# Optimization experiments

Hardware: AMD Instinct MI355X
Metric: run time of the kernel (lower is better)

## Reference

```python
import jax, jax.numpy as jnp
import numpy as np

N_NODES = 100000
N_EDGES = 1600000
IN_SIZE = 128
HIDDEN = 128
OUT_SIZE = 64


def setup_inputs() -> dict:
    key = jax.random.key(0)
    k = jax.random.split(key, 8)
    feat = jax.random.normal(k[0], (N_NODES, IN_SIZE), dtype=jnp.float32)
    src = jax.random.randint(k[1], (N_EDGES,), 0, N_NODES, dtype=jnp.int32)
    dst = jax.random.randint(k[2], (N_EDGES,), 0, N_NODES, dtype=jnp.int32)
    # fc_neigh weights for the two SAGEConv layers (stored as [in, out])
    W1 = jax.random.normal(k[3], (IN_SIZE, HIDDEN), dtype=jnp.float32) / np.sqrt(IN_SIZE)
    b1 = jnp.zeros((HIDDEN,), dtype=jnp.float32)
    W2 = jax.random.normal(k[4], (HIDDEN, OUT_SIZE), dtype=jnp.float32) / np.sqrt(HIDDEN)
    b2 = jnp.zeros((OUT_SIZE,), dtype=jnp.float32)
    return {"feat": feat, "W1": W1, "b1": b1, "W2": W2, "b2": b2,
            "src": src, "dst": dst}


def _sage_gcn(h, src, dst, W, b):
    # DGL SAGEConv with aggregator_type='gcn':
    #   neigh = segment_sum over incoming edges of src features
    #   h_neigh = (neigh + h_self) / (in_degree + 1)
    #   out = h_neigh @ W + b   (fc_self is not used for 'gcn')
    neigh = jax.ops.segment_sum(h[src], dst, num_segments=N_NODES)  # [N, d]
    deg = jax.ops.segment_sum(jnp.ones((src.shape[0],), dtype=h.dtype), dst,
                              num_segments=N_NODES)                 # [N]
    h_neigh = (neigh + h) / (deg + 1.0)[:, None]
    return h_neigh @ W + b


def reference(feat, W1, b1, W2, b2, src, dst):
    # dropout(p=0.0) is identity; activation between layers only
    h = _sage_gcn(feat, src, dst, W1, b1)
    h = jax.nn.relu(h)
    h = _sage_gcn(h, src, dst, W2, b2)
    return h
```

## Files before the change

kernel.cpp:

```cpp
#include <hip/hip_runtime.h>

#define NNODES 100000
#define NEDGES 1600000
#define BSHIFT 7
#define NB 782
#define CAP 2560
#define EBLOCKS 391
#define GEMM_BLOCKS 1563

typedef _Float16 f16;
typedef _Float16 v8h __attribute__((ext_vector_type(8)));
typedef float v4f __attribute__((ext_vector_type(4)));

#if __has_builtin(__builtin_amdgcn_cvt_f32_ubyte0)
#define CVTB0(u) __builtin_amdgcn_cvt_f32_ubyte0(u)
#define CVTB1(u) __builtin_amdgcn_cvt_f32_ubyte1(u)
#define CVTB2(u) __builtin_amdgcn_cvt_f32_ubyte2(u)
#define CVTB3(u) __builtin_amdgcn_cvt_f32_ubyte3(u)
#else
#define CVTB0(u) ((float)((u) & 0xFFu))
#define CVTB1(u) ((float)(((u) >> 8) & 0xFFu))
#define CVTB2(u) ((float)(((u) >> 16) & 0xFFu))
#define CVTB3(u) ((float)((u) >> 24))
#endif

__device__ inline void acc8(float s, uint2 u, float* a) {
    a[0] = fmaf(s, CVTB0(u.x), a[0]);
    a[1] = fmaf(s, CVTB1(u.x), a[1]);
    a[2] = fmaf(s, CVTB2(u.x), a[2]);
    a[3] = fmaf(s, CVTB3(u.x), a[3]);
    a[4] = fmaf(s, CVTB0(u.y), a[4]);
    a[5] = fmaf(s, CVTB1(u.y), a[5]);
    a[6] = fmaf(s, CVTB2(u.y), a[6]);
    a[7] = fmaf(s, CVTB3(u.y), a[7]);
}

__global__ __launch_bounds__(256) void init_k(int* __restrict__ bcur,
                                              const float* __restrict__ W1,
                                              f16* __restrict__ W1t,
                                              const float* __restrict__ W2,
                                              f16* __restrict__ W2t) {
    int t = blockIdx.x * 256 + threadIdx.x;
    if (t < NB) bcur[t] = t * CAP;
    int u = t - 1024;
    if (u >= 0) {
        if (u < 128 * 128) {
            int k = u >> 7, n = u & 127;
            W1t[n * 128 + k] = (f16)W1[k * 128 + n];
        } else if (u < 128 * 128 + 128 * 64) {
            int v = u - 128 * 128;
            int k = v >> 6, n = v & 63;
            W2t[n * 128 + k] = (f16)W2[k * 64 + n];
        }
    }
}

__global__ __launch_bounds__(256) void scatter_gemm1(
    const int* __restrict__ src, const int* __restrict__ dst,
    int* __restrict__ bcur, int* __restrict__ ebuf,
    const float* __restrict__ feat, const f16* __restrict__ W1t,
    unsigned char* __restrict__ z1, float* __restrict__ sc1) {
    constexpr int PITCH = 136;
    __shared__ __align__(16) char smem[128 * PITCH * 2];
    int tid = threadIdx.x;

    if (blockIdx.x < EBLOCKS) {
        int* h = (int*)smem;
        int* base_s = ((int*)smem) + 1024;
        for (int i = tid; i < NB; i += 256) h[i] = 0;
        __syncthreads();
        int base = blockIdx.x * 4096;
        int d[16], sv[16];
        for (int k = 0; k < 16; k++) {
            int e = base + k * 256 + tid;
            if (e < NEDGES) {
                d[k] = dst[e];
                sv[k] = src[e];
                atomicAdd(&h[d[k] >> BSHIFT], 1);
            } else {
                d[k] = -1;
            }
        }
        __syncthreads();
        for (int i = tid; i < NB; i += 256) {
            int c = h[i];
            if (c) base_s[i] = atomicAdd(&bcur[i], c);
            h[i] = 0;
        }
        __syncthreads();
        for (int k = 0; k < 16; k++) {
            if (d[k] >= 0) {
                int b = d[k] >> BSHIFT;
                int slot = atomicAdd(&h[b], 1);
                ebuf[base_s[b] + slot] = sv[k] | ((d[k] & 127) << 24);
            }
        }
        return;
    }

    f16* wlds = (f16*)smem;
    for (int c = tid; c < 128 * 16; c += 256) {
        int n = c >> 4;
        int kc = c & 15;
        *(v8h*)&wlds[n * PITCH + kc * 8] = *(const v8h*)&W1t[n * 128 + kc * 8];
    }
    __syncthreads();

    int wave = tid >> 6, lane = tid & 63, quad = lane >> 4, l16 = lane & 15;
    int m0 = (blockIdx.x - EBLOCKS) * 64 + wave * 16;
    if (m0 >= NNODES) return;

    v8h a[4];
    const float* arow = feat + (long)(m0 + l16) * 128 + quad * 8;
#pragma unroll
    for (int kb = 0; kb < 4; kb++) {
        float4 f0 = *(const float4*)(arow + kb * 32);
        float4 f1 = *(const float4*)(arow + kb * 32 + 4);
        v8h t = {(f16)f0.x, (f16)f0.y, (f16)f0.z, (f16)f0.w,
                 (f16)f1.x, (f16)f1.y, (f16)f1.z, (f16)f1.w};
        a[kb] = t;
    }

    v4f acc[8];
#pragma unroll
    for (int nt = 0; nt < 8; nt++) {
        v4f c4 = {0.f, 0.f, 0.f, 0.f};
        const f16* brow = &wlds[(nt * 16 + l16) * PITCH + quad * 8];
#pragma unroll
        for (int kb = 0; kb < 4; kb++) {
            v8h b = *(const v8h*)(brow + kb * 32);
            c4 = __builtin_amdgcn_mfma_f32_16x16x32_f16(a[kb], b, c4, 0, 0, 0);
        }
        acc[nt] = c4;
    }

#pragma unroll
    for (int r = 0; r < 4; r++) {
        float m = 0.f;
#pragma unroll
        for (int nt = 0; nt < 8; nt++) m = fmaxf(m, fabsf(acc[nt][r]));
        m = fmaxf(m, __shfl_xor(m, 1));
        m = fmaxf(m, __shfl_xor(m, 2));
        m = fmaxf(m, __shfl_xor(m, 4));
        m = fmaxf(m, __shfl_xor(m, 8));
        int row = m0 + quad * 4 + r;
        float rs = (m > 0.f) ? 127.f / m : 0.f;
        if (l16 == 0) sc1[row] = (m > 0.f) ? m / 127.f : 0.f;
#pragma unroll
        for (int nt = 0; nt < 8; nt++) {
            int qv = (int)rintf(acc[nt][r] * rs) + 128;
            z1[(long)row * 128 + nt * 16 + l16] = (unsigned char)qv;
        }
    }
}

__global__ __launch_bounds__(256) void fill_bucket(const int* __restrict__ ebuf,
                                                   const int* __restrict__ bcur,
                                                   const float* __restrict__ sc1,
                                                   int* __restrict__ begs,
                                                   int* __restrict__ ends,
                                                   int2* __restrict__ csr8) {
    __shared__ int lc[128];
    __shared__ int ls[256];
    int b = blockIdx.x;
    int tid = threadIdx.x;
    if (tid < 128) lc[tid] = 0;
    __syncthreads();
    int ebeg = b * CAP;
    int eend = bcur[b];
    for (int e = ebeg + tid; e < eend; e += 256)
        atomicAdd(&lc[((unsigned)ebuf[e]) >> 24], 1);
    __syncthreads();
    int cnt = (tid < 128) ? lc[tid] : 0;
    ls[tid] = cnt;
    __syncthreads();
    for (int off = 1; off < 256; off <<= 1) {
        int t = (tid >= off) ? ls[tid - off] : 0;
        __syncthreads();
        ls[tid] += t;
        __syncthreads();
    }
    int excl = ls[tid] - cnt;
    int node = (b << BSHIFT) + tid;
    if (tid < 128 && node < NNODES) {
        begs[node] = ebeg + excl;
        ends[node] = ebeg + excl + cnt;
    }
    if (tid < 128) { ls[tid] = excl; lc[tid] = 0; }
    __syncthreads();
    for (int e = ebeg + tid; e < eend; e += 256) {
        int p = ebuf[e];
        int dloc = ((unsigned)p) >> 24;
        int s = p & 0xFFFFFF;
        int slot = atomicAdd(&lc[dloc], 1);
        csr8[ebeg + ls[dloc] + slot] = make_int2(s, __float_as_int(sc1[s]));
    }
}

__global__ __launch_bounds__(256, 8) void gather128_h1(
    const unsigned char* __restrict__ z,
    const float* __restrict__ sc,
    const int2* __restrict__ csr8,
    const int* __restrict__ begs, const int* __restrict__ ends,
    const float* __restrict__ b1,
    f16* __restrict__ h1)
{
    int tid = threadIdx.x;
    int c = tid & 15;
    int node = blockIdx.x * 16 + (tid >> 4);

    int beg = begs[node];
    int end = ends[node];

    unsigned coff = (unsigned)c << 3;

    float a[8];
#pragma unroll
    for (int j = 0; j < 8; j++) a[j] = 0.f;
    float ssum = 0.f;

    {
        float s = sc[node];
        uint2 u = *(const uint2*)(z + (((unsigned)node) << 7) + coff);
        ssum += s;
        acc8(s, u, a);
    }

    int e = beg;
    while (__any(e < end)) {
        int2 q0 = {0, 0}, q1 = {0, 0}, q2 = {0, 0}, q3 = {0, 0};
        int2 q4 = {0, 0}, q5 = {0, 0}, q6 = {0, 0}, q7 = {0, 0};
        if (e     < end) q0 = csr8[e];
        if (e + 1 < end) q1 = csr8[e + 1];
        if (e + 2 < end) q2 = csr8[e + 2];
        if (e + 3 < end) q3 = csr8[e + 3];
        if (e + 4 < end) q4 = csr8[e + 4];
        if (e + 5 < end) q5 = csr8[e + 5];
        if (e + 6 < end) q6 = csr8[e + 6];
        if (e + 7 < end) q7 = csr8[e + 7];
        uint2 u0 = make_uint2(0, 0), u1 = make_uint2(0, 0);
        uint2 u2 = make_uint2(0, 0), u3 = make_uint2(0, 0);
        uint2 u4 = make_uint2(0, 0), u5 = make_uint2(0, 0);
        uint2 u6 = make_uint2(0, 0), u7 = make_uint2(0, 0);
        if (e     < end) u0 = *(const uint2*)(z + (((unsigned)q0.x) << 7) + coff);
        if (e + 1 < end) u1 = *(const uint2*)(z + (((unsigned)q1.x) << 7) + coff);
        if (e + 2 < end) u2 = *(const uint2*)(z + (((unsigned)q2.x) << 7) + coff);
        if (e + 3 < end) u3 = *(const uint2*)(z + (((unsigned)q3.x) << 7) + coff);
        if (e + 4 < end) u4 = *(const uint2*)(z + (((unsigned)q4.x) << 7) + coff);
        if (e + 5 < end) u5 = *(const uint2*)(z + (((unsigned)q5.x) << 7) + coff);
        if (e + 6 < end) u6 = *(const uint2*)(z + (((unsigned)q6.x) << 7) + coff);
        if (e + 7 < end) u7 = *(const uint2*)(z + (((unsigned)q7.x) << 7) + coff);
        float s0 = __int_as_float(q0.y), s1 = __int_as_float(q1.y);
        float s2 = __int_as_float(q2.y), s3 = __int_as_float(q3.y);
        float s4 = __int_as_float(q4.y), s5 = __int_as_float(q5.y);
        float s6 = __int_as_float(q6.y), s7 = __int_as_float(q7.y);
        ssum += ((s0 + s1) + (s2 + s3)) + ((s4 + s5) + (s6 + s7));
        acc8(s0, u0, a); acc8(s1, u1, a); acc8(s2, u2, a); acc8(s3, u3, a);
        acc8(s4, u4, a); acc8(s5, u5, a); acc8(s6, u6, a); acc8(s7, u7, a);
        e += 8;
    }

    {
        float base = 128.f * ssum;
        float inv = 1.0f / (float)(end - beg + 1);
        float4 bb0 = ((const float4*)b1)[c * 2];
        float4 bb1 = ((const float4*)b1)[c * 2 + 1];
        v8h o = {(f16)fmaxf((a[0] - base) * inv + bb0.x, 0.f),
                 (f16)fmaxf((a[1] - base) * inv + bb0.y, 0.f),
                 (f16)fmaxf((a[2] - base) * inv + bb0.z, 0.f),
                 (f16)fmaxf((a[3] - base) * inv + bb0.w, 0.f),
                 (f16)fmaxf((a[4] - base) * inv + bb1.x, 0.f),
                 (f16)fmaxf((a[5] - base) * inv + bb1.y, 0.f),
                 (f16)fmaxf((a[6] - base) * inv + bb1.z, 0.f),
                 (f16)fmaxf((a[7] - base) * inv + bb1.w, 0.f)};
        *(v8h*)&h1[(long)node * 128 + c * 8] = o;
    }
}

__global__ __launch_bounds__(256) void gemm2_k(
    const f16* __restrict__ h1,
    const f16* __restrict__ W2t,
    unsigned char* __restrict__ z2,
    float* __restrict__ sc2)
{
    constexpr int PITCH = 136;
    __shared__ f16 wlds[64 * PITCH];
    int tid = threadIdx.x;
    for (int c = tid; c < 64 * 16; c += 256) {
        int n = c >> 4;
        int kc = c & 15;
        *(v8h*)&wlds[n * PITCH + kc * 8] = *(const v8h*)&W2t[n * 128 + kc * 8];
    }
    __syncthreads();

    int wave = tid >> 6, lane = tid & 63, quad = lane >> 4, l16 = lane & 15;
    int m0 = blockIdx.x * 64 + wave * 16;
    if (m0 >= NNODES) return;

    v8h a[4];
    const f16* arow = h1 + (long)(m0 + l16) * 128 + quad * 8;
#pragma unroll
    for (int kb = 0; kb < 4; kb++) a[kb] = *(const v8h*)(arow + kb * 32);

    v4f acc[4];
#pragma unroll
    for (int nt = 0; nt < 4; nt++) {
        v4f c4 = {0.f, 0.f, 0.f, 0.f};
        const f16* brow = &wlds[(nt * 16 + l16) * PITCH + quad * 8];
#pragma unroll
        for (int kb = 0; kb < 4; kb++) {
            v8h b = *(const v8h*)(brow + kb * 32);
            c4 = __builtin_amdgcn_mfma_f32_16x16x32_f16(a[kb], b, c4, 0, 0, 0);
        }
        acc[nt] = c4;
    }

#pragma unroll
    for (int r = 0; r < 4; r++) {
        float m = 0.f;
#pragma unroll
        for (int nt = 0; nt < 4; nt++) m = fmaxf(m, fabsf(acc[nt][r]));
        m = fmaxf(m, __shfl_xor(m, 1));
        m = fmaxf(m, __shfl_xor(m, 2));
        m = fmaxf(m, __shfl_xor(m, 4));
        m = fmaxf(m, __shfl_xor(m, 8));
        int row = m0 + quad * 4 + r;
        float rs = (m > 0.f) ? 127.f / m : 0.f;
        if (l16 == 0) sc2[row] = (m > 0.f) ? m / 127.f : 0.f;
#pragma unroll
        for (int nt = 0; nt < 4; nt++) {
            int qv = (int)rintf(acc[nt][r] * rs) + 128;
            z2[(long)row * 64 + nt * 16 + l16] = (unsigned char)qv;
        }
    }
}

__global__ __launch_bounds__(256, 8) void gather64(
    const unsigned char* __restrict__ z, const float* __restrict__ sc,
    const int2* __restrict__ csr8,
    const int* __restrict__ begs, const int* __restrict__ ends,
    const float* __restrict__ bias, float4* __restrict__ out) {
    int tid = threadIdx.x;
    int lane = tid & 63;
    int c = lane & 7;
    int node = blockIdx.x * 32 + (tid >> 3);

    int beg = begs[node];
    int end = ends[node];

    unsigned coff = (unsigned)c << 3;

    float a[8];
#pragma unroll
    for (int j = 0; j < 8; j++) a[j] = 0.f;
    float ssum = 0.f;

    {
        float s = sc[node];
        uint2 u = *(const uint2*)(z + (((unsigned)node) << 6) + coff);
        ssum += s;
        acc8(s, u, a);
    }

    int e = beg;
    while (__any(e < end)) {
        float s0 = 0.f, s1 = 0.f, s2 = 0.f, s3 = 0.f;
        float s4 = 0.f, s5 = 0.f, s6 = 0.f, s7 = 0.f;
        uint2 u0 = make_uint2(0, 0), u1 = make_uint2(0, 0);
        uint2 u2 = make_uint2(0, 0), u3 = make_uint2(0, 0);
        uint2 u4 = make_uint2(0, 0), u5 = make_uint2(0, 0);
        uint2 u6 = make_uint2(0, 0), u7 = make_uint2(0, 0);
        if (e     < end) { int i = csr8[e    ].x; s0 = sc[i]; u0 = *(const uint2*)(z + (((unsigned)i) << 6) + coff); }
        if (e + 1 < end) { int i = csr8[e + 1].x; s1 = sc[i]; u1 = *(const uint2*)(z + (((unsigned)i) << 6) + coff); }
        if (e + 2 < end) { int i = csr8[e + 2].x; s2 = sc[i]; u2 = *(const uint2*)(z + (((unsigned)i) << 6) + coff); }
        if (e + 3 < end) { int i = csr8[e + 3].x; s3 = sc[i]; u3 = *(const uint2*)(z + (((unsigned)i) << 6) + coff); }
        if (e + 4 < end) { int i = csr8[e + 4].x; s4 = sc[i]; u4 = *(const uint2*)(z + (((unsigned)i) << 6) + coff); }
        if (e + 5 < end) { int i = csr8[e + 5].x; s5 = sc[i]; u5 = *(const uint2*)(z + (((unsigned)i) << 6) + coff); }
        if (e + 6 < end) { int i = csr8[e + 6].x; s6 = sc[i]; u6 = *(const uint2*)(z + (((unsigned)i) << 6) + coff); }
        if (e + 7 < end) { int i = csr8[e + 7].x; s7 = sc[i]; u7 = *(const uint2*)(z + (((unsigned)i) << 6) + coff); }
        ssum += ((s0 + s1) + (s2 + s3)) + ((s4 + s5) + (s6 + s7));
        acc8(s0, u0, a); acc8(s1, u1, a); acc8(s2, u2, a); acc8(s3, u3, a);
        acc8(s4, u4, a); acc8(s5, u5, a); acc8(s6, u6, a); acc8(s7, u7, a);
        e += 8;
    }

    {
        float base = 128.f * ssum;
        float inv = 1.0f / (float)(end - beg + 1);
        float4 b0 = ((const float4*)bias)[c * 2];
        float4 b1v = ((const float4*)bias)[c * 2 + 1];
        out[(long)node * 16 + c * 2] =
            make_float4((a[0] - base) * inv + b0.x, (a[1] - base) * inv + b0.y,
                        (a[2] - base) * inv + b0.z, (a[3] - base) * inv + b0.w);
        out[(long)node * 16 + c * 2 + 1] =
            make_float4((a[4] - base) * inv + b1v.x, (a[5] - base) * inv + b1v.y,
                        (a[6] - base) * inv + b1v.z, (a[7] - base) * inv + b1v.w);
    }
}

extern "C" void kernel_launch(void* const* d_in, const int* in_sizes, int n_in,
                              void* d_out, int out_size, void* d_ws, size_t ws_size,
                              hipStream_t stream) {
    const float* feat = (const float*)d_in[0];
    const float* W1   = (const float*)d_in[1];
    const float* b1   = (const float*)d_in[2];
    const float* W2   = (const float*)d_in[3];
    const float* b2   = (const float*)d_in[4];
    const int*   src  = (const int*)d_in[5];
    const int*   dst  = (const int*)d_in[6];
    float* out = (float*)d_out;

    char* ws = (char*)d_ws;
    int* bcur = (int*)(ws + 0x0000000);
    int* begs = (int*)(ws + 0x0001000);
    int* ends = (int*)(ws + 0x0063000);
    int* ebuf = (int*)(ws + 0x00C5000);
    int2* csr8 = (int2*)(ws + 0x0900000);
    unsigned char* z1 = (unsigned char*)(ws + 0x1900000);
    float* sc1 = (float*)(ws + 0x2600000);
    f16* h1   = (f16*)(ws + 0x2700000);
    unsigned char* z2 = (unsigned char*)(ws + 0x4100000);
    float* sc2 = (float*)(ws + 0x4800000);
    f16* W1t  = (f16*)(ws + 0x4900000);
    f16* W2t  = (f16*)(ws + 0x4910000);

    init_k<<<100, 256, 0, stream>>>(bcur, W1, W1t, W2, W2t);

    scatter_gemm1<<<EBLOCKS + GEMM_BLOCKS, 256, 0, stream>>>(src, dst, bcur, ebuf,
                                                             feat, W1t, z1, sc1);

    fill_bucket<<<NB, 256, 0, stream>>>(ebuf, bcur, sc1, begs, ends, csr8);

    gather128_h1<<<NNODES / 16, 256, 0, stream>>>(z1, sc1, csr8, begs, ends,
                                                  b1, h1);

    gemm2_k<<<GEMM_BLOCKS, 256, 0, stream>>>(h1, W2t, z2, sc2);

    gather64<<<3125, 256, 0, stream>>>(z2, sc2, csr8, begs, ends, b2,
                                       (float4*)out);
}
```

Measured before the change: 249.9 us.

## Switch int8 quantization from per-row to per-column scales with integer gather accumulation

Replaces per-row int8 scales with per-column scales found through a global atomicMax over each GEMM's output. The scale can then be applied once after aggregation, so the gathers sum packed bytes with plain integer adds instead of float FMAs. The CSR shrinks from int2 to int4, and scale loads per edge are gone. In exchange, the GEMMs now write fp16 intermediates and separate quantize passes (merged into fill_quant, plus quant_z2) add extra memory traffic and launches. Per-column scales may also lose accuracy compared with per-row scales.

```diff
diff --git a/kernel.cpp b/kernel.cpp
--- a/kernel.cpp
+++ b/kernel.cpp
@@ -7,41 +7,31 @@
 #define CAP 2560
 #define EBLOCKS 391
 #define GEMM_BLOCKS 1563
+#define QBLOCKS 6250
 
 typedef _Float16 f16;
 typedef _Float16 v8h __attribute__((ext_vector_type(8)));
 typedef float v4f __attribute__((ext_vector_type(4)));
 
-#if __has_builtin(__builtin_amdgcn_cvt_f32_ubyte0)
-#define CVTB0(u) __builtin_amdgcn_cvt_f32_ubyte0(u)
-#define CVTB1(u) __builtin_amdgcn_cvt_f32_ubyte1(u)
-#define CVTB2(u) __builtin_amdgcn_cvt_f32_ubyte2(u)
-#define CVTB3(u) __builtin_amdgcn_cvt_f32_ubyte3(u)
-#else
-#define CVTB0(u) ((float)((u) & 0xFFu))
-#define CVTB1(u) ((float)(((u) >> 8) & 0xFFu))
-#define CVTB2(u) ((float)(((u) >> 16) & 0xFFu))
-#define CVTB3(u) ((float)((u) >> 24))
-#endif
-
-__device__ inline void acc8(float s, uint2 u, float* a) {
-    a[0] = fmaf(s, CVTB0(u.x), a[0]);
-    a[1] = fmaf(s, CVTB1(u.x), a[1]);
-    a[2] = fmaf(s, CVTB2(u.x), a[2]);
-    a[3] = fmaf(s, CVTB3(u.x), a[3]);
-    a[4] = fmaf(s, CVTB0(u.y), a[4]);
-    a[5] = fmaf(s, CVTB1(u.y), a[5]);
-    a[6] = fmaf(s, CVTB2(u.y), a[6]);
-    a[7] = fmaf(s, CVTB3(u.y), a[7]);
+__device__ inline void accu(uint2 u, unsigned& A, unsigned& B,
+                            unsigned& C, unsigned& D) {
+    A += u.x & 0x00FF00FFu;
+    B += (u.x >> 8) & 0x00FF00FFu;
+    C += u.y & 0x00FF00FFu;
+    D += (u.y >> 8) & 0x00FF00FFu;
 }
 
 __global__ __launch_bounds__(256) void init_k(int* __restrict__ bcur,
                                               const float* __restrict__ W1,
                                               f16* __restrict__ W1t,
                                               const float* __restrict__ W2,
-                                              f16* __restrict__ W2t) {
+                                              f16* __restrict__ W2t,
+                                              int* __restrict__ colmax1,
+                                              int* __restrict__ colmax2) {
     int t = blockIdx.x * 256 + threadIdx.x;
     if (t < NB) bcur[t] = t * CAP;
+    if (t >= 800 && t < 928) colmax1[t - 800] = 0;
+    if (t >= 928 && t < 992) colmax2[t - 928] = 0;
     int u = t - 1024;
     if (u >= 0) {
         if (u < 128 * 128) {
@@ -59,9 +49,10 @@
     const int* __restrict__ src, const int* __restrict__ dst,
     int* __restrict__ bcur, int* __restrict__ ebuf,
     const float* __restrict__ feat, const f16* __restrict__ W1t,
-    unsigned char* __restrict__ z1, float* __restrict__ sc1) {
+    f16* __restrict__ z1f, int* __restrict__ colmax1) {
     constexpr int PITCH = 136;
     __shared__ __align__(16) char smem[128 * PITCH * 2];
+    __shared__ int lmax[128];
     int tid = threadIdx.x;
 
     if (blockIdx.x < EBLOCKS) {
@@ -104,14 +95,17 @@
         int kc = c & 15;
         *(v8h*)&wlds[n * PITCH + kc * 8] = *(const v8h*)&W1t[n * 128 + kc * 8];
     }
+    if (tid < 128) lmax[tid] = 0;
     __syncthreads();
 
     int wave = tid >> 6, lane = tid & 63, quad = lane >> 4, l16 = lane & 15;
     int m0 = (blockIdx.x - EBLOCKS) * 64 + wave * 16;
-    if (m0 >= NNODES) return;
+    bool valid = (m0 < NNODES);
+    int mrow = m0 + l16;
+    if (mrow >= NNODES) mrow = NNODES - 1;
 
     v8h a[4];
-    const float* arow = feat + (long)(m0 + l16) * 128 + quad * 8;
+    const float* arow = feat + (long)mrow * 128 + quad * 8;
 #pragma unroll
     for (int kb = 0; kb < 4; kb++) {
         float4 f0 = *(const float4*)(arow + kb * 32);
@@ -121,7 +115,6 @@
         a[kb] = t;
     }
 
-    v4f acc[8];
 #pragma unroll
     for (int nt = 0; nt < 8; nt++) {
         v4f c4 = {0.f, 0.f, 0.f, 0.f};
@@ -131,178 +124,187 @@
             v8h b = *(const v8h*)(brow + kb * 32);
             c4 = __builtin_amdgcn_mfma_f32_16x16x32_f16(a[kb], b, c4, 0, 0, 0);
         }
-        acc[nt] = c4;
-    }
-
-#pragma unroll
-    for (int r = 0; r < 4; r++) {
-        float m = 0.f;
-#pragma unroll
-        for (int nt = 0; nt < 8; nt++) m = fmaxf(m, fabsf(acc[nt][r]));
-        m = fmaxf(m, __shfl_xor(m, 1));
-        m = fmaxf(m, __shfl_xor(m, 2));
-        m = fmaxf(m, __shfl_xor(m, 4));
-        m = fmaxf(m, __shfl_xor(m, 8));
-        int row = m0 + quad * 4 + r;
-        float rs = (m > 0.f) ? 127.f / m : 0.f;
-        if (l16 == 0) sc1[row] = (m > 0.f) ? m / 127.f : 0.f;
-#pragma unroll
-        for (int nt = 0; nt < 8; nt++) {
-            int qv = (int)rintf(acc[nt][r] * rs) + 128;
-            z1[(long)row * 128 + nt * 16 + l16] = (unsigned char)qv;
-        }
-    }
-}
-
-__global__ __launch_bounds__(256) void fill_bucket(const int* __restrict__ ebuf,
-                                                   const int* __restrict__ bcur,
-                                                   const float* __restrict__ sc1,
-                                                   int* __restrict__ begs,
-                                                   int* __restrict__ ends,
-                                                   int2* __restrict__ csr8) {
+        int n = nt * 16 + l16;
+        if (valid) {
+#pragma unroll
+            for (int r = 0; r < 4; r++)
+                z1f[(long)(m0 + quad * 4 + r) * 128 + n] = (f16)c4[r];
+        }
+        float m = fmaxf(fmaxf(fabsf(c4[0]), fabsf(c4[1])),
+                        fmaxf(fabsf(c4[2]), fabsf(c4[3])));
+        m = fmaxf(m, __shfl_xor(m, 16));
+        m = fmaxf(m, __shfl_xor(m, 32));
+        if (quad == 0) atomicMax(&lmax[n], __float_as_int(m));
+    }
+    __syncthreads();
+    if (tid < 128) atomicMax(&colmax1[tid], lmax[tid]);
+}
+
+__global__ __launch_bounds__(256) void fill_quant(const int* __restrict__ ebuf,
+                                                  const int* __restrict__ bcur,
+                                                  int* __restrict__ begs,
+                                                  int* __restrict__ ends,
+                                                  int* __restrict__ csr4,
+                                                  const f16* __restrict__ z1f,
+                                                  const int* __restrict__ colmax1,
+                                                  unsigned char* __restrict__ z1q) {
     __shared__ int lc[128];
     __shared__ int ls[256];
-    int b = blockIdx.x;
-    int tid = threadIdx.x;
-    if (tid < 128) lc[tid] = 0;
-    __syncthreads();
-    int ebeg = b * CAP;
-    int eend = bcur[b];
-    for (int e = ebeg + tid; e < eend; e += 256)
-        atomicAdd(&lc[((unsigned)ebuf[e]) >> 24], 1);
-    __syncthreads();
-    int cnt = (tid < 128) ? lc[tid] : 0;
-    ls[tid] = cnt;
-    __syncthreads();
-    for (int off = 1; off < 256; off <<= 1) {
-        int t = (tid >= off) ? ls[tid - off] : 0;
-        __syncthreads();
-        ls[tid] += t;
-        __syncthreads();
-    }
-    int excl = ls[tid] - cnt;
-    int node = (b << BSHIFT) + tid;
-    if (tid < 128 && node < NNODES) {
-        begs[node] = ebeg + excl;
-        ends[node] = ebeg + excl + cnt;
-    }
-    if (tid < 128) { ls[tid] = excl; lc[tid] = 0; }
-    __syncthreads();
-    for (int e = ebeg + tid; e < eend; e += 256) {
-        int p = ebuf[e];
-        int dloc = ((unsigned)p) >> 24;
-        int s = p & 0xFFFFFF;
-        int slot = atomicAdd(&lc[dloc], 1);
-        csr8[ebeg + ls[dloc] + slot] = make_int2(s, __float_as_int(sc1[s]));
-    }
+    __shared__ float rs[128];
+    int tid = threadIdx.x;
+
+    if (blockIdx.x < NB) {
+        int b = blockIdx.x;
+        if (tid < 128) lc[tid] = 0;
+        __syncthreads();
+        int ebeg = b * CAP;
+        int eend = bcur[b];
+        for (int e = ebeg + tid; e < eend; e += 256)
+            atomicAdd(&lc[((unsigned)ebuf[e]) >> 24], 1);
+        __syncthreads();
+        int cnt = (tid < 128) ? lc[tid] : 0;
+        ls[tid] = cnt;
+        __syncthreads();
+        for (int off = 1; off < 256; off <<= 1) {
+            int t = (tid >= off) ? ls[tid - off] : 0;
+            __syncthreads();
+            ls[tid] += t;
+            __syncthreads();
+        }
+        int excl = ls[tid] - cnt;
+        int node = (b << BSHIFT) + tid;
+        if (tid < 128 && node < NNODES) {
+            begs[node] = ebeg + excl;
+            ends[node] = ebeg + excl + cnt;
+        }
+        if (tid < 128) { ls[tid] = excl; lc[tid] = 0; }
+        __syncthreads();
+        for (int e = ebeg + tid; e < eend; e += 256) {
+            int p = ebuf[e];
+            int dloc = ((unsigned)p) >> 24;
+            int slot = atomicAdd(&lc[dloc], 1);
+            csr4[ebeg + ls[dloc] + slot] = p & 0xFFFFFF;
+        }
+        return;
+    }
+
+    if (tid < 128) {
+        float m = __int_as_float(colmax1[tid]);
+        rs[tid] = (m > 0.f) ? 127.f / m : 0.f;
+    }
+    __syncthreads();
+    long base = (long)(blockIdx.x - NB) * 2048 + tid * 8;
+    v8h v = *(const v8h*)&z1f[base];
+    int c0 = (int)(base & 127);
+    unsigned q[8];
+#pragma unroll
+    for (int j = 0; j < 8; j++)
+        q[j] = (unsigned)((int)rintf((float)v[j] * rs[c0 + j]) + 128);
+    uint2 o;
+    o.x = q[0] | (q[1] << 8) | (q[2] << 16) | (q[3] << 24);
+    o.y = q[4] | (q[5] << 8) | (q[6] << 16) | (q[7] << 24);
+    *(uint2*)&z1q[base] = o;
 }
 
 __global__ __launch_bounds__(256, 8) void gather128_h1(
     const unsigned char* __restrict__ z,
-    const float* __restrict__ sc,
-    const int2* __restrict__ csr8,
+    const int* __restrict__ csr,
     const int* __restrict__ begs, const int* __restrict__ ends,
+    const int* __restrict__ colmax1,
     const float* __restrict__ b1,
-    f16* __restrict__ h1)
-{
+    f16* __restrict__ h1) {
     int tid = threadIdx.x;
     int c = tid & 15;
     int node = blockIdx.x * 16 + (tid >> 4);
 
     int beg = begs[node];
     int end = ends[node];
-
     unsigned coff = (unsigned)c << 3;
 
-    float a[8];
-#pragma unroll
-    for (int j = 0; j < 8; j++) a[j] = 0.f;
-    float ssum = 0.f;
-
+    unsigned A = 0, B = 0, C = 0, D = 0;
     {
-        float s = sc[node];
         uint2 u = *(const uint2*)(z + (((unsigned)node) << 7) + coff);
-        ssum += s;
-        acc8(s, u, a);
+        accu(u, A, B, C, D);
     }
 
     int e = beg;
     while (__any(e < end)) {
-        int2 q0 = {0, 0}, q1 = {0, 0}, q2 = {0, 0}, q3 = {0, 0};
-        int2 q4 = {0, 0}, q5 = {0, 0}, q6 = {0, 0}, q7 = {0, 0};
-        if (e     < end) q0 = csr8[e];
-        if (e + 1 < end) q1 = csr8[e + 1];
-        if (e + 2 < end) q2 = csr8[e + 2];
-        if (e + 3 < end) q3 = csr8[e + 3];
-        if (e + 4 < end) q4 = csr8[e + 4];
-        if (e + 5 < end) q5 = csr8[e + 5];
-        if (e + 6 < end) q6 = csr8[e + 6];
-        if (e + 7 < end) q7 = csr8[e + 7];
+        int i0 = 0, i1 = 0, i2 = 0, i3 = 0, i4 = 0, i5 = 0, i6 = 0, i7 = 0;
+        if (e     < end) i0 = csr[e];
+        if (e + 1 < end) i1 = csr[e + 1];
+        if (e + 2 < end) i2 = csr[e + 2];
+        if (e + 3 < end) i3 = csr[e + 3];
+        if (e + 4 < end) i4 = csr[e + 4];
+        if (e + 5 < end) i5 = csr[e + 5];
+        if (e + 6 < end) i6 = csr[e + 6];
+        if (e + 7 < end) i7 = csr[e + 7];
         uint2 u0 = make_uint2(0, 0), u1 = make_uint2(0, 0);
         uint2 u2 = make_uint2(0, 0), u3 = make_uint2(0, 0);
         uint2 u4 = make_uint2(0, 0), u5 = make_uint2(0, 0);
         uint2 u6 = make_uint2(0, 0), u7 = make_uint2(0, 0);
-        if (e     < end) u0 = *(const uint2*)(z + (((unsigned)q0.x) << 7) + coff);
-        if (e + 1 < end) u1 = *(const uint2*)(z + (((unsigned)q1.x) << 7) + coff);
-        if (e + 2 < end) u2 = *(const uint2*)(z + (((unsigned)q2.x) << 7) + coff);
-        if (e + 3 < end) u3 = *(const uint2*)(z + (((unsigned)q3.x) << 7) + coff);
-        if (e + 4 < end) u4 = *(const uint2*)(z + (((unsigned)q4.x) << 7) + coff);
-        if (e + 5 < end) u5 = *(const uint2*)(z + (((unsigned)q5.x) << 7) + coff);
-        if (e + 6 < end) u6 = *(const uint2*)(z + (((unsigned)q6.x) << 7) + coff);
-        if (e + 7 < end) u7 = *(const uint2*)(z + (((unsigned)q7.x) << 7) + coff);
-        float s0 = __int_as_float(q0.y), s1 = __int_as_float(q1.y);
-        float s2 = __int_as_float(q2.y), s3 = __int_as_float(q3.y);
-        float s4 = __int_as_float(q4.y), s5 = __int_as_float(q5.y);
-        float s6 = __int_as_float(q6.y), s7 = __int_as_float(q7.y);
-        ssum += ((s0 + s1) + (s2 + s3)) + ((s4 + s5) + (s6 + s7));
-        acc8(s0, u0, a); acc8(s1, u1, a); acc8(s2, u2, a); acc8(s3, u3, a);
-        acc8(s4, u4, a); acc8(s5, u5, a); acc8(s6, u6, a); acc8(s7, u7, a);
+        if (e     < end) u0 = *(const uint2*)(z + (((unsigned)i0) << 7) + coff);
+        if (e + 1 < end) u1 = *(const uint2*)(z + (((unsigned)i1) << 7) + coff);
+        if (e + 2 < end) u2 = *(const uint2*)(z + (((unsigned)i2) << 7) + coff);
+        if (e + 3 < end) u3 = *(const uint2*)(z + (((unsigned)i3) << 7) + coff);
+        if (e + 4 < end) u4 = *(const uint2*)(z + (((unsigned)i4) << 7) + coff);
+        if (e + 5 < end) u5 = *(const uint2*)(z + (((unsigned)i5) << 7) + coff);
+        if (e + 6 < end) u6 = *(const uint2*)(z + (((unsigned)i6) << 7) + coff);
+        if (e + 7 < end) u7 = *(const uint2*)(z + (((unsigned)i7) << 7) + coff);
+        accu(u0, A, B, C, D); accu(u1, A, B, C, D);
+        accu(u2, A, B, C, D); accu(u3, A, B, C, D);
+        accu(u4, A, B, C, D); accu(u5, A, B, C, D);
+        accu(u6, A, B, C, D); accu(u7, A, B, C, D);
         e += 8;
     }
 
-    {
-        float base = 128.f * ssum;
-        float inv = 1.0f / (float)(end - beg + 1);
-        float4 bb0 = ((const float4*)b1)[c * 2];
-        float4 bb1 = ((const float4*)b1)[c * 2 + 1];
-        v8h o = {(f16)fmaxf((a[0] - base) * inv + bb0.x, 0.f),
-                 (f16)fmaxf((a[1] - base) * inv + bb0.y, 0.f),
-                 (f16)fmaxf((a[2] - base) * inv + bb0.z, 0.f),
-                 (f16)fmaxf((a[3] - base) * inv + bb0.w, 0.f),
-                 (f16)fmaxf((a[4] - base) * inv + bb1.x, 0.f),
-                 (f16)fmaxf((a[5] - base) * inv + bb1.y, 0.f),
-                 (f16)fmaxf((a[6] - base) * inv + bb1.z, 0.f),
-                 (f16)fmaxf((a[7] - base) * inv + bb1.w, 0.f)};
-        *(v8h*)&h1[(long)node * 128 + c * 8] = o;
-    }
+    int cnt = end - beg + 1;
+    int b128 = 128 * cnt;
+    int is[8];
+    is[0] = (int)(A & 0xFFFFu); is[2] = (int)(A >> 16);
+    is[1] = (int)(B & 0xFFFFu); is[3] = (int)(B >> 16);
+    is[4] = (int)(C & 0xFFFFu); is[6] = (int)(C >> 16);
+    is[5] = (int)(D & 0xFFFFu); is[7] = (int)(D >> 16);
+    float inv = 1.0f / (float)cnt;
+    float4 bb0 = ((const float4*)b1)[c * 2];
+    float4 bb1 = ((const float4*)b1)[c * 2 + 1];
+    float bv[8] = {bb0.x, bb0.y, bb0.z, bb0.w, bb1.x, bb1.y, bb1.z, bb1.w};
+    v8h o;
+#pragma unroll
+    for (int j = 0; j < 8; j++) {
+        float s = __int_as_float(colmax1[c * 8 + j]) * (1.0f / 127.0f) * inv;
+        o[j] = (f16)fmaxf((float)(is[j] - b128) * s + bv[j], 0.f);
+    }
+    *(v8h*)&h1[(long)node * 128 + c * 8] = o;
 }
 
 __global__ __launch_bounds__(256) void gemm2_k(
     const f16* __restrict__ h1,
     const f16* __restrict__ W2t,
-    unsigned char* __restrict__ z2,
-    float* __restrict__ sc2)
-{
+    f16* __restrict__ z2f,
+    int* __restrict__ colmax2) {
     constexpr int PITCH = 136;
     __shared__ f16 wlds[64 * PITCH];
+    __shared__ int lmax[64];
     int tid = threadIdx.x;
     for (int c = tid; c < 64 * 16; c += 256) {
         int n = c >> 4;
         int kc = c & 15;
         *(v8h*)&wlds[n * PITCH + kc * 8] = *(const v8h*)&W2t[n * 128 + kc * 8];
     }
+    if (tid < 64) lmax[tid] = 0;
     __syncthreads();
 
     int wave = tid >> 6, lane = tid & 63, quad = lane >> 4, l16 = lane & 15;
     int m0 = blockIdx.x * 64 + wave * 16;
-    if (m0 >= NNODES) return;
+    bool valid = (m0 < NNODES);
+    int mrow = m0 + l16;
+    if (mrow >= NNODES) mrow = NNODES - 1;
 
     v8h a[4];
-    const f16* arow = h1 + (long)(m0 + l16) * 128 + quad * 8;
+    const f16* arow = h1 + (long)mrow * 128 + quad * 8;
 #pragma unroll
     for (int kb = 0; kb < 4; kb++) a[kb] = *(const v8h*)(arow + kb * 32);
 
-    v4f acc[4];
 #pragma unroll
     for (int nt = 0; nt < 4; nt++) {
         v4f c4 = {0.f, 0.f, 0.f, 0.f};
@@ -312,90 +314,114 @@
             v8h b = *(const v8h*)(brow + kb * 32);
             c4 = __builtin_amdgcn_mfma_f32_16x16x32_f16(a[kb], b, c4, 0, 0, 0);
         }
-        acc[nt] = c4;
-    }
-
-#pragma unroll
-    for (int r = 0; r < 4; r++) {
-        float m = 0.f;
-#pragma unroll
-        for (int nt = 0; nt < 4; nt++) m = fmaxf(m, fabsf(acc[nt][r]));
-        m = fmaxf(m, __shfl_xor(m, 1));
-        m = fmaxf(m, __shfl_xor(m, 2));
-        m = fmaxf(m, __shfl_xor(m, 4));
-        m = fmaxf(m, __shfl_xor(m, 8));
-        int row = m0 + quad * 4 + r;
-        float rs = (m > 0.f) ? 127.f / m : 0.f;
-        if (l16 == 0) sc2[row] = (m > 0.f) ? m / 127.f : 0.f;
-#pragma unroll
-        for (int nt = 0; nt < 4; nt++) {
-            int qv = (int)rintf(acc[nt][r] * rs) + 128;
-            z2[(long)row * 64 + nt * 16 + l16] = (unsigned char)qv;
-        }
-    }
+        int n = nt * 16 + l16;
+        if (valid) {
+#pragma unroll
+            for (int r = 0; r < 4; r++)
+                z2f[(long)(m0 + quad * 4 + r) * 64 + n] = (f16)c4[r];
+        }
+        float m = fmaxf(fmaxf(fabsf(c4[0]), fabsf(c4[1])),
+                        fmaxf(fabsf(c4[2]), fabsf(c4[3])));
+        m = fmaxf(m, __shfl_xor(m, 16));
+        m = fmaxf(m, __shfl_xor(m, 32));
+        if (quad == 0) atomicMax(&lmax[n], __float_as_int(m));
+    }
+    __syncthreads();
+    if (tid < 64) atomicMax(&colmax2[tid], lmax[tid]);
+}
+
+__global__ __launch_bounds__(256) void quant_z2(const f16* __restrict__ z2f,
+                                                const int* __restrict__ colmax2,
+                                                unsigned char* __restrict__ z2q) {
+    __shared__ float rs[64];
+    int tid = threadIdx.x;
+    if (tid < 64) {
+        float m = __int_as_float(colmax2[tid]);
+        rs[tid] = (m > 0.f) ? 127.f / m : 0.f;
+    }
+    __syncthreads();
+    long base = (long)blockIdx.x * 2048 + tid * 8;
+    v8h v = *(const v8h*)&z2f[base];
+    int c0 = (int)(base & 63);
+    unsigned q[8];
+#pragma unroll
+    for (int j = 0; j < 8; j++)
+        q[j] = (unsigned)((int)rintf((float)v[j] * rs[c0 + j]) + 128);
+    uint2 o;
+    o.x = q[0] | (q[1] << 8) | (q[2] << 16) | (q[3] << 24);
+    o.y = q[4] | (q[5] << 8) | (q[6] << 16) | (q[7] << 24);
+    *(uint2*)&z2q[base] = o;
 }
 
 __global__ __launch_bounds__(256, 8) void gather64(
-    const unsigned char* __restrict__ z, const float* __restrict__ sc,
-    const int2* __restrict__ csr8,
+    const unsigned char* __restrict__ z, const int* __restrict__ csr,
     const int* __restrict__ begs, const int* __restrict__ ends,
+    const int* __restrict__ colmax2,
     const float* __restrict__ bias, float4* __restrict__ out) {
     int tid = threadIdx.x;
-    int lane = tid & 63;
-    int c = lane & 7;
+    int c = tid & 7;
     int node = blockIdx.x * 32 + (tid >> 3);
 
     int beg = begs[node];
     int end = ends[node];
-
     unsigned coff = (unsigned)c << 3;
 
-    float a[8];
-#pragma unroll
-    for (int j = 0; j < 8; j++) a[j] = 0.f;
-    float ssum = 0.f;
-
+    unsigned A = 0, B = 0, C = 0, D = 0;
     {
-        float s = sc[node];
         uint2 u = *(const uint2*)(z + (((unsigned)node) << 6) + coff);
-        ssum += s;
-        acc8(s, u, a);
+        accu(u, A, B, C, D);
     }
 
     int e = beg;
     while (__any(e < end)) {
-        float s0 = 0.f, s1 = 0.f, s2 = 0.f, s3 = 0.f;
-        float s4 = 0.f, s5 = 0.f, s6 = 0.f, s7 = 0.f;
+        int i0 = 0, i1 = 0, i2 = 0, i3 = 0, i4 = 0, i5 = 0, i6 = 0, i7 = 0;
+        if (e     < end) i0 = csr[e];
+        if (e + 1 < end) i1 = csr[e + 1];
+        if (e + 2 < end) i2 = csr[e + 2];
+        if (e + 3 < end) i3 = csr[e + 3];
+        if (e + 4 < end) i4 = csr[e + 4];
+        if (e + 5 < end) i5 = csr[e + 5];
+        if (e + 6 < end) i6 = csr[e + 6];
+        if (e + 7 < end) i7 = csr[e + 7];
         uint2 u0 = make_uint2(0, 0), u1 = make_uint2(0, 0);
         uint2 u2 = make_uint2(0, 0), u3 = make_uint2(0, 0);
         uint2 u4 = make_uint2(0, 0), u5 = make_uint2(0, 0);
         uint2 u6 = make_uint2(0, 0), u7 = make_uint2(0, 0);
-        if (e     < end) { int i = csr8[e    ].x; s0 = sc[i]; u0 = *(const uint2*)(z + (((unsigned)i) << 6) + coff); }
-        if (e + 1 < end) { int i = csr8[e + 1].x; s1 = sc[i]; u1 = *(const uint2*)(z + (((unsigned)i) << 6) + coff); }
-        if (e + 2 < end) { int i = csr8[e + 2].x; s2 = sc[i]; u2 = *(const uint2*)(z + (((unsigned)i) << 6) + coff); }
-        if (e + 3 < end) { int i = csr8[e + 3].x; s3 = sc[i]; u3 = *(const uint2*)(z + (((unsigned)i) << 6) + coff); }
-        if (e + 4 < end) { int i = csr8[e + 4].x; s4 = sc[i]; u4 = *(const uint2*)(z + (((unsigned)i) << 6) + coff); }
-        if (e + 5 < end) { int i = csr8[e + 5].x; s5 = sc[i]; u5 = *(const uint2*)(z + (((unsigned)i) << 6) + coff); }
-        if (e + 6 < end) { int i = csr8[e + 6].x; s6 = sc[i]; u6 = *(const uint2*)(z + (((unsigned)i) << 6) + coff); }
-        if (e + 7 < end) { int i = csr8[e + 7].x; s7 = sc[i]; u7 = *(const uint2*)(z + (((unsigned)i) << 6) + coff); }
-        ssum += ((s0 + s1) + (s2 + s3)) + ((s4 + s5) + (s6 + s7));
-        acc8(s0, u0, a); acc8(s1, u1, a); acc8(s2, u2, a); acc8(s3, u3, a);
-        acc8(s4, u4, a); acc8(s5, u5, a); acc8(s6, u6, a); acc8(s7, u7, a);
+        if (e     < end) u0 = *(const uint2*)(z + (((unsigned)i0) << 6) + coff);
+        if (e + 1 < end) u1 = *(const uint2*)(z + (((unsigned)i1) << 6) + coff);
+        if (e + 2 < end) u2 = *(const uint2*)(z + (((unsigned)i2) << 6) + coff);
+        if (e + 3 < end) u3 = *(const uint2*)(z + (((unsigned)i3) << 6) + coff);
+        if (e + 4 < end) u4 = *(const uint2*)(z + (((unsigned)i4) << 6) + coff);
+        if (e + 5 < end) u5 = *(const uint2*)(z + (((unsigned)i5) << 6) + coff);
+        if (e + 6 < end) u6 = *(const uint2*)(z + (((unsigned)i6) << 6) + coff);
+        if (e + 7 < end) u7 = *(const uint2*)(z + (((unsigned)i7) << 6) + coff);
+        accu(u0, A, B, C, D); accu(u1, A, B, C, D);
+        accu(u2, A, B, C, D); accu(u3, A, B, C, D);
+        accu(u4, A, B, C, D); accu(u5, A, B, C, D);
+        accu(u6, A, B, C, D); accu(u7, A, B, C, D);
         e += 8;
     }
 
-    {
-        float base = 128.f * ssum;
-        float inv = 1.0f / (float)(end - beg + 1);
-        float4 b0 = ((const float4*)bias)[c * 2];
-        float4 b1v = ((const float4*)bias)[c * 2 + 1];
-        out[(long)node * 16 + c * 2] =
-            make_float4((a[0] - base) * inv + b0.x, (a[1] - base) * inv + b0.y,
-                        (a[2] - base) * inv + b0.z, (a[3] - base) * inv + b0.w);
-        out[(long)node * 16 + c * 2 + 1] =
-            make_float4((a[4] - base) * inv + b1v.x, (a[5] - base) * inv + b1v.y,
-                        (a[6] - base) * inv + b1v.z, (a[7] - base) * inv + b1v.w);
-    }
+    int cnt = end - beg + 1;
+    int b128 = 128 * cnt;
+    int is[8];
+    is[0] = (int)(A & 0xFFFFu); is[2] = (int)(A >> 16);
+    is[1] = (int)(B & 0xFFFFu); is[3] = (int)(B >> 16);
+    is[4] = (int)(C & 0xFFFFu); is[6] = (int)(C >> 16);
+    is[5] = (int)(D & 0xFFFFu); is[7] = (int)(D >> 16);
+    float inv = 1.0f / (float)cnt;
+    float4 b0 = ((const float4*)bias)[c * 2];
+    float4 b1v = ((const float4*)bias)[c * 2 + 1];
+    float r[8];
+#pragma unroll
+    for (int j = 0; j < 8; j++) {
+        float s = __int_as_float(colmax2[c * 8 + j]) * (1.0f / 127.0f) * inv;
+        r[j] = (float)(is[j] - b128) * s;
+    }
+    out[(long)node * 16 + c * 2] =
+        make_float4(r[0] + b0.x, r[1] + b0.y, r[2] + b0.z, r[3] + b0.w);
+    out[(long)node * 16 + c * 2 + 1] =
+        make_float4(r[4] + b1v.x, r[5] + b1v.y, r[6] + b1v.z, r[7] + b1v.w);
 }
 
 extern "C" void kernel_launch(void* const* d_in, const int* in_sizes, int n_in,
@@ -411,31 +437,37 @@
     float* out = (float*)d_out;
 
     char* ws = (char*)d_ws;
-    int* bcur = (int*)(ws + 0x0000000);
-    int* begs = (int*)(ws + 0x0001000);
-    int* ends = (int*)(ws + 0x0063000);
-    int* ebuf = (int*)(ws + 0x00C5000);
-    int2* csr8 = (int2*)(ws + 0x0900000);
-    unsigned char* z1 = (unsigned char*)(ws + 0x1900000);
-    float* sc1 = (float*)(ws + 0x2600000);
-    f16* h1   = (f16*)(ws + 0x2700000);
-    unsigned char* z2 = (unsigned char*)(ws + 0x4100000);
-    float* sc2 = (float*)(ws + 0x4800000);
-    f16* W1t  = (f16*)(ws + 0x4900000);
-    f16* W2t  = (f16*)(ws + 0x4910000);
-
-    init_k<<<100, 256, 0, stream>>>(bcur, W1, W1t, W2, W2t);
+    int* bcur    = (int*)(ws + 0x0000000);
+    int* colmax1 = (int*)(ws + 0x0001000);
+    int* colmax2 = (int*)(ws + 0x0001400);
+    int* begs    = (int*)(ws + 0x0002000);
+    int* ends    = (int*)(ws + 0x0064000);
+    int* ebuf    = (int*)(ws + 0x00C8000);
+    int* csr4    = (int*)(ws + 0x0900000);
+    f16* z1f     = (f16*)(ws + 0x1100000);
+    f16* h1      = (f16*)(ws + 0x1100000);
+    unsigned char* z1q = (unsigned char*)(ws + 0x2A00000);
+    f16* z2f     = (f16*)(ws + 0x3700000);
+    unsigned char* z2q = (unsigned char*)(ws + 0x4400000);
+    f16* W1t     = (f16*)(ws + 0x4B00000);
+    f16* W2t     = (f16*)(ws + 0x4B10000);
+
+    init_k<<<100, 256, 0, stream>>>(bcur, W1, W1t, W2, W2t, colmax1, colmax2);
 
     scatter_gemm1<<<EBLOCKS + GEMM_BLOCKS, 256, 0, stream>>>(src, dst, bcur, ebuf,
-                                                             feat, W1t, z1, sc1);
-
-    fill_bucket<<<NB, 256, 0, stream>>>(ebuf, bcur, sc1, begs, ends, csr8);
-
-    gather128_h1<<<NNODES / 16, 256, 0, stream>>>(z1, sc1, csr8, begs, ends,
-                                                  b1, h1);
-
-    gemm2_k<<<GEMM_BLOCKS, 256, 0, stream>>>(h1, W2t, z2, sc2);
-
-    gather64<<<3125, 256, 0, stream>>>(z2, sc2, csr8, begs, ends, b2,
+                                                             feat, W1t, z1f,
+                                                             colmax1);
+
+    fill_quant<<<NB + QBLOCKS, 256, 0, stream>>>(ebuf, bcur, begs, ends, csr4,
+                                                 z1f, colmax1, z1q);
+
+    gather128_h1<<<NNODES / 16, 256, 0, stream>>>(z1q, csr4, begs, ends,
+                                                  colmax1, b1, h1);
+
+    gemm2_k<<<GEMM_BLOCKS, 256, 0, stream>>>(h1, W2t, z2f, colmax2);
+
+    quant_z2<<<3125, 256, 0, stream>>>(z2f, colmax2, z2q);
+
+    gather64<<<3125, 256, 0, stream>>>(z2q, csr4, begs, ends, colmax2, b2,
                                        (float4*)out);
 }
```

Result: slower. 270.7 us (+8.3%).
